# Kernel optimization log

Measured on AMD Instinct MI355X. Metric: run time of the kernel, lower is better.

The kernel has to match this reference:

```python
import jax, jax.numpy as jnp
import numpy as np

TYPE_NUM = 4
CHILDS = [2, 2, 2, 2]
NODE_NUM = 8          # sum(CHILDS)
HEADS = 4
GROUP = 4
IN, MID, OUT = 256, 256, 256


def _mask():
    m = np.zeros((TYPE_NUM, NODE_NUM), np.float32)
    s = 0
    for i, c in enumerate(CHILDS):
        m[i, s:s + c] = 1.0
        s += c
    return jnp.asarray(m)


def _graph_feature(x, node_num):
    # x: [B, L, C] -> [B, M, node_num+1, C] with M = (L-1)//node_num
    B, L, C = x.shape
    node_x = x[:, 1:, :].reshape(B, -1, C * node_num)
    M = node_x.shape[1]
    src = x[:, :M, :]
    return jnp.concatenate([node_x, src], axis=2).reshape(B, M, node_num + 1, C)


def _conv1d(x, w, b, groups):
    # x: [N, C, T], w: [O, C//groups, K], stride == K, 'VALID' -> length-1 output
    y = jax.lax.conv_general_dilated(
        x, w, window_strides=(w.shape[-1],), padding='VALID',
        feature_group_count=groups, dimension_numbers=('NCH', 'OIH', 'NCH'))
    return y + b[None, :, None]


def _agg(feat, attn, mask):
    # feat: [B, M, node_num+1, C]; attn: [B, M, node_num, HEADS] (softmaxed)
    B, M, A, C = feat.shape
    n = A - 1
    nf = feat[:, :, :-1, :].reshape(B, M, n, HEADS, C // HEADS) * attn[..., None]
    nf = nf.reshape(B, M, n, C)
    agg = jnp.einsum('tn,bmnc->bmtc', mask, nf)  # masked group-sum (bmm with block mask)
    return agg, feat[:, :, -1, :]


def setup_inputs() -> dict:
    key = jax.random.key(0)
    ks = jax.random.split(key, 12)
    B, L = 4, 32777

    def lin(k, fi, fo):
        return jax.random.normal(k, (fi, fo), jnp.float32) / np.sqrt(fi).astype(np.float32)

    def convw(k, o, i, kk):
        return jax.random.normal(k, (o, i, kk), jnp.float32) / np.sqrt(i * kk).astype(np.float32)

    return {
        'input': jax.random.normal(ks[0], (B, L, IN), jnp.float32),
        'gt': jax.random.normal(ks[1], (B, 512, IN), jnp.float32),
        'w_att': lin(ks[2], IN, HEADS), 'b_att': jnp.zeros((HEADS,), jnp.float32),
        'w_gt1': lin(ks[3], IN, MID), 'b_gt1': jnp.zeros((MID,), jnp.float32),
        'w_gt2': lin(ks[4], MID, OUT), 'b_gt2': jnp.zeros((OUT,), jnp.float32),
        'w_agg1': convw(ks[5], MID, IN // GROUP, TYPE_NUM), 'b_agg1': jnp.zeros((MID,), jnp.float32),
        'w_src1': convw(ks[6], MID, IN // GROUP, 1), 'b_src1': jnp.zeros((MID,), jnp.float32),
        'w_agg2': convw(ks[7], OUT, MID // GROUP, TYPE_NUM), 'b_agg2': jnp.zeros((OUT,), jnp.float32),
        'w_src2': convw(ks[8], OUT, MID // GROUP, 1), 'b_src2': jnp.zeros((OUT,), jnp.float32),
    }


def reference(input, gt, w_att, b_att, w_gt1, b_gt1, w_gt2, b_gt2,
              w_agg1, b_agg1, w_src1, b_src1, w_agg2, b_agg2, w_src2, b_src2):
    mask = _mask()
    B = gt.shape[0]
    # gt branch (eval mode: dropout = identity)
    gt1 = jax.nn.relu(gt @ w_gt1 + b_gt1)   # [B, 512, MID]
    gt2 = jax.nn.relu(gt1 @ w_gt2 + b_gt2)  # [B, 512, OUT]

    # ---- layer 1 ----
    feat = _graph_feature(input, NODE_NUM)   # [B, M, 9, IN]
    M = feat.shape[1]
    ft = feat[:, :, -1:, :] + feat[:, :, :-1, :]          # source + each neighbor
    attn = jax.nn.softmax(ft @ w_att + b_att, axis=2)     # softmax over node dim
    node, src = _agg(feat, attn, mask)                    # [B,M,T,IN], [B,M,IN]
    BM = B * M
    node = jnp.transpose(node.reshape(BM, TYPE_NUM, IN), (0, 2, 1))  # [BM, IN, T]
    src = src.reshape(BM, IN, 1)
    node1 = jax.nn.relu(_conv1d(node, w_agg1, b_agg1, GROUP))[:, :, 0]  # [BM, MID]
    src1 = jax.nn.relu(_conv1d(src, w_src1, b_src1, GROUP))[:, :, 0]

    nf1 = node1.reshape(B, M, MID)[:, 0, :]
    d1 = gt1[:, 0, :] - nf1
    score1 = 1.0 - jnp.exp(-0.5 * jnp.sum(d1 * d1, axis=1))  # [B]

    out1 = (node1 + src1).reshape(B, M, MID)

    # ---- layer 2 (reuses attn truncated to M2) ----
    feat2 = _graph_feature(out1, NODE_NUM)  # [B, M2, 9, MID]
    M2 = feat2.shape[1]
    node2, src2 = _agg(feat2, attn[:, :M2], mask)
    BM2 = B * M2
    node2 = jnp.transpose(node2.reshape(BM2, TYPE_NUM, MID), (0, 2, 1))
    src2 = src2.reshape(BM2, MID, 1)
    node2c = jax.nn.relu(_conv1d(node2, w_agg2, b_agg2, GROUP))  # [BM2, OUT, 1]

    nf2 = node2c.reshape(B, M2, OUT)
    d2 = (gt2[:, :M2, :] - nf2).reshape(-1, OUT)
    score2 = 1.0 - jnp.exp(-0.5 * jnp.sum(d2 * d2, axis=1))  # [B*M2]

    src2c = jax.nn.relu(_conv1d(src2, w_src2, b_src2, GROUP))
    output = (node2c + src2c).reshape(-1, OUT)  # [B*M2, OUT]
    return output, score1, score2
```

## Files before the change

kernel.cpp:

```cpp
#include <hip/hip_runtime.h>
#include <hip/hip_bf16.h>

typedef unsigned short u16;
typedef unsigned int   u32;
typedef __attribute__((ext_vector_type(8))) short short8;
typedef __attribute__((ext_vector_type(4))) float f32x4;

#define BB  4
#define LL  32777
#define MM  4097
#define MMP 4112
#define MM2 512

__device__ __forceinline__ float b2f(u16 u) { return __uint_as_float(((u32)u) << 16); }
__device__ __forceinline__ u16 f2bf(float f) {
    u32 u = __float_as_uint(f);
    return (u16)((u + 0x7fffu + ((u >> 16) & 1u)) >> 16);
}
__device__ __forceinline__ u32 pk(float a, float b) {
    union { __hip_bfloat162 h; u32 u; } cv;
    cv.h = __float22bfloat162_rn(make_float2(a, b));
    return cv.u;
}
__device__ __forceinline__ float bflo(u32 u) { return __uint_as_float(u << 16); }
__device__ __forceinline__ float bfhi(u32 u) { return __uint_as_float(u & 0xffff0000u); }

__global__ __launch_bounds__(256) void setup_k(
    const float* __restrict__ wagg1, const float* __restrict__ wagg2,
    const float* __restrict__ wsrc1, const float* __restrict__ wsrc2,
    const float* __restrict__ watt,
    u16* __restrict__ wA1, u16* __restrict__ wA2,
    u16* __restrict__ wS1, u16* __restrict__ wS2, u16* __restrict__ wattB) {
    int idx = blockIdx.x * 256 + threadIdx.x;
    if (idx < 131072) {
        int which = idx >> 16;
        int e = idx & 65535;
        int j = e & 7, lane = (e >> 3) & 63, mt = (e >> 9) & 3, kc = (e >> 11) & 7, g = (e >> 14) & 3;
        int ol = mt * 16 + (lane & 15);
        int k = kc * 32 + (lane >> 4) * 8 + j;
        int t = k >> 6, ci = k & 63;
        const float* src = which ? wagg2 : wagg1;
        u16* dst = which ? wA2 : wA1;
        dst[e] = f2bf(src[(g * 64 + ol) * 256 + ci * 4 + t]);
    } else if (idx < 163840) {
        int e2 = idx - 131072;
        int which = e2 >> 14;
        int e = e2 & 16383;
        int j = e & 7, lane = (e >> 3) & 63, mt = (e >> 9) & 3, kc = (e >> 11) & 1, g = (e >> 12) & 3;
        int ol = mt * 16 + (lane & 15);
        int k = kc * 32 + (lane >> 4) * 8 + j;
        const float* src = which ? wsrc2 : wsrc1;
        u16* dst = which ? wS2 : wS1;
        dst[e] = f2bf(src[(g * 64 + ol) * 64 + k]);
    } else {
        int e = idx - 163840;
        int j = e & 7, lane = (e >> 3) & 63, kc = e >> 9;
        int h = lane & 15, quad = lane >> 4;
        int k = kc * 32 + quad * 8 + j;
        wattB[e] = (h < 4) ? f2bf(watt[k * 4 + h]) : (u16)0;
    }
}

__global__ __launch_bounds__(256, 4) void l1fused_k(
    const float* __restrict__ x, const float* __restrict__ batt,
    const u16* __restrict__ wA1, const u16* __restrict__ wS1,
    const u16* __restrict__ wattB,
    const float* __restrict__ bagg1, const float* __restrict__ bsrc1,
    float* __restrict__ attnf, u16* __restrict__ out1, float* __restrict__ n1m0,
    const float* __restrict__ gt, const float* __restrict__ W1, const float* __restrict__ b1,
    const float* __restrict__ W2, const float* __restrict__ b2,
    float* __restrict__ gt2, float* __restrict__ gt1m0) {
    __shared__ u16   sh_node[64 * 256];
    __shared__ u16   sh_srcq[8 * 256];
    __shared__ float shR[320];

    int tid = threadIdx.x;
    int b = blockIdx.y;

    if (blockIdx.x < 64) {
        float (*sh)[8] = (float(*)[8])sh_node;
        int gi = blockIdx.x * 4 + b;
        int row0 = gi * 8;
        {
            int r = tid >> 5, j = tid & 31;
            const float4* a4 = (const float4*)(gt + (size_t)(row0 + r) * 256 + j * 8);
            float4 v0 = a4[0], v1 = a4[1];
            sh[j * 8 + 0][r] = v0.x; sh[j * 8 + 1][r] = v0.y;
            sh[j * 8 + 2][r] = v0.z; sh[j * 8 + 3][r] = v0.w;
            sh[j * 8 + 4][r] = v1.x; sh[j * 8 + 5][r] = v1.y;
            sh[j * 8 + 6][r] = v1.z; sh[j * 8 + 7][r] = v1.w;
        }
        __syncthreads();
        int o = tid;
        float acc[8];
        {
            float bo = b1[o];
            #pragma unroll
            for (int i = 0; i < 8; ++i) acc[i] = bo;
        }
        #pragma unroll 8
        for (int k = 0; k < 256; ++k) {
            float wv = W1[k * 256 + o];
            const float4* ap = (const float4*)&sh[k][0];
            float4 a0 = ap[0], a1 = ap[1];
            acc[0] = fmaf(a0.x, wv, acc[0]); acc[1] = fmaf(a0.y, wv, acc[1]);
            acc[2] = fmaf(a0.z, wv, acc[2]); acc[3] = fmaf(a0.w, wv, acc[3]);
            acc[4] = fmaf(a1.x, wv, acc[4]); acc[5] = fmaf(a1.y, wv, acc[5]);
            acc[6] = fmaf(a1.z, wv, acc[6]); acc[7] = fmaf(a1.w, wv, acc[7]);
        }
        #pragma unroll
        for (int i = 0; i < 8; ++i) acc[i] = fmaxf(acc[i], 0.f);
        if ((row0 & 511) == 0) gt1m0[(row0 >> 9) * 256 + o] = acc[0];
        __syncthreads();
        #pragma unroll
        for (int i = 0; i < 8; ++i) sh[o][i] = acc[i];
        __syncthreads();
        {
            float bo = b2[o];
            #pragma unroll
            for (int i = 0; i < 8; ++i) acc[i] = bo;
        }
        #pragma unroll 8
        for (int k = 0; k < 256; ++k) {
            float wv = W2[k * 256 + o];
            const float4* ap = (const float4*)&sh[k][0];
            float4 a0 = ap[0], a1 = ap[1];
            acc[0] = fmaf(a0.x, wv, acc[0]); acc[1] = fmaf(a0.y, wv, acc[1]);
            acc[2] = fmaf(a0.z, wv, acc[2]); acc[3] = fmaf(a0.w, wv, acc[3]);
            acc[4] = fmaf(a1.x, wv, acc[4]); acc[5] = fmaf(a1.y, wv, acc[5]);
            acc[6] = fmaf(a1.z, wv, acc[6]); acc[7] = fmaf(a1.w, wv, acc[7]);
        }
        #pragma unroll
        for (int i = 0; i < 8; ++i) gt2[(size_t)(row0 + i) * 256 + o] = fmaxf(acc[i], 0.f);
        return;
    }

    int bx = blockIdx.x - 64;
    int lane = tid & 63, w = tid >> 6;
    int quad = lane >> 4;
    int p0 = bx * 8;

    {
        int rslot = tid >> 4, cseg = tid & 15;
        const float* xb = x + (size_t)b * LL * 256;
        const float* srcA[5];
        u16* dstA[5];
        int keyA[5];
        #pragma unroll
        for (int pass = 0; pass < 5; ++pass) {
            int r = pass * 16 + rslot;
            int grow, key; u16* dst;
            if (r < 64) {
                int pos = r >> 3, nn = r & 7;
                int gp = p0 + pos; int gpc = gp < MM ? gp : MM - 1;
                grow = 1 + 8 * gpc + nn;
                dst = sh_node + r * 256;
                key = (pos ^ nn) & 7;
            } else {
                int q = r - 64;
                int qq = q < 8 ? q : 7;
                int gp = p0 + qq; int gpc = gp < MM ? gp : MM - 1;
                grow = gpc;
                dst = sh_srcq + qq * 256;
                key = qq & 7;
            }
            srcA[pass] = xb + (size_t)grow * 256 + cseg * 16;
            dstA[pass] = dst;
            keyA[pass] = key;
        }
        float4 v0[5], v1[5], v2[5], v3[5];
        #pragma unroll
        for (int pass = 0; pass < 5; ++pass) {
            asm volatile("global_load_dwordx4 %0, %1, off"           : "=v"(v0[pass]) : "v"(srcA[pass]));
            asm volatile("global_load_dwordx4 %0, %1, off offset:16" : "=v"(v1[pass]) : "v"(srcA[pass]));
            asm volatile("global_load_dwordx4 %0, %1, off offset:32" : "=v"(v2[pass]) : "v"(srcA[pass]));
            asm volatile("global_load_dwordx4 %0, %1, off offset:48" : "=v"(v3[pass]) : "v"(srcA[pass]));
        }
        asm volatile("s_waitcnt vmcnt(0)" ::: "memory");
        __builtin_amdgcn_sched_barrier(0);
        #pragma unroll
        for (int pass = 0; pass < 5; ++pass) {
            bool val = (pass < 4) || (rslot < 8);
            if (val) {
                uint4 o0, o1;
                o0.x = pk(v0[pass].x, v0[pass].y); o0.y = pk(v0[pass].z, v0[pass].w);
                o0.z = pk(v1[pass].x, v1[pass].y); o0.w = pk(v1[pass].z, v1[pass].w);
                o1.x = pk(v2[pass].x, v2[pass].y); o1.y = pk(v2[pass].z, v2[pass].w);
                o1.z = pk(v3[pass].x, v3[pass].y); o1.w = pk(v3[pass].z, v3[pass].w);
                int cb0 = cseg * 2, key = keyA[pass];
                *(uint4*)(dstA[pass] + ((cb0 ^ key) * 8))       = o0;
                *(uint4*)(dstA[pass] + (((cb0 + 1) ^ key) * 8)) = o1;
            }
        }
    }
    short8 wB[8];
    #pragma unroll
    for (int kc = 0; kc < 8; ++kc) wB[kc] = *(const short8*)(wattB + kc * 512 + lane * 8);
    float battw = batt[w];
    __syncthreads();

    {
        int m = lane & 15;
        int h = lane & 15;
        {
            int r = w * 16 + m;
            int key = ((r >> 3) ^ (r & 7)) & 7;
            const u16* rowp = sh_node + r * 256;
            f32x4 acc = (f32x4){0.f, 0.f, 0.f, 0.f};
            #pragma unroll
            for (int kc = 0; kc < 8; ++kc) {
                int cb = kc * 4 + quad;
                short8 aF = *(const short8*)(rowp + ((cb ^ key) * 8));
                acc = __builtin_amdgcn_mfma_f32_16x16x32_bf16(aF, wB[kc], acc, 0, 0, 0);
            }
            if (h < 4) {
                #pragma unroll
                for (int r2 = 0; r2 < 4; ++r2)
                    shR[(w * 16 + quad * 4 + r2) * 4 + h] = acc[r2];
            }
        }
        if (w == 3) {
            int ms = m < 8 ? m : 7;
            int key = ms & 7;
            const u16* rowp = sh_srcq + ms * 256;
            f32x4 acc = (f32x4){0.f, 0.f, 0.f, 0.f};
            #pragma unroll
            for (int kc = 0; kc < 8; ++kc) {
                int cb = kc * 4 + quad;
                short8 aF = *(const short8*)(rowp + ((cb ^ key) * 8));
                acc = __builtin_amdgcn_mfma_f32_16x16x32_bf16(aF, wB[kc], acc, 0, 0, 0);
            }
            if (h < 4) {
                #pragma unroll
                for (int r2 = 0; r2 < 4; ++r2) {
                    int rr = quad * 4 + r2;
                    if (rr < 8) shR[256 + rr * 4 + h] = acc[r2];
                }
            }
        }
    }
    __syncthreads();

    int g = w;
    int col = lane & 15;
    int pos = col & 7;
    float aT[8];
    {
        float base = shR[256 + pos * 4 + g] + battw;
        float l[8], mx = -3.0e38f;
        #pragma unroll
        for (int n = 0; n < 8; ++n) { l[n] = shR[(pos * 8 + n) * 4 + g] + base; mx = fmaxf(mx, l[n]); }
        float s = 0.f;
        #pragma unroll
        for (int n = 0; n < 8; ++n) { l[n] = __expf(l[n] - mx); s += l[n]; }
        float inv = 1.f / s;
        #pragma unroll
        for (int n = 0; n < 8; ++n) aT[n] = l[n] * inv;
        int gp = p0 + pos;
        if (quad == 0 && col < 8 && gp < MM2) {
            #pragma unroll
            for (int n = 0; n < 8; ++n)
                attnf[(((size_t)b * MM2 + gp) * 8 + n) * 4 + g] = aT[n];
        }
    }
    f32x4 accn[4], accs[4];
    #pragma unroll
    for (int mt = 0; mt < 4; ++mt) { accn[mt] = (f32x4){0,0,0,0}; accs[mt] = (f32x4){0,0,0,0}; }

    const u16* wAb = wA1 + (size_t)(g * 8) * 4 * 512 + lane * 8;
    short8 aAc[4];
    #pragma unroll
    for (int mt = 0; mt < 4; ++mt) aAc[mt] = *(const short8*)(wAb + mt * 512);

    #pragma unroll
    for (int kc = 0; kc < 8; ++kc) {
        short8 aAn[4];
        if (kc < 7) {
            #pragma unroll
            for (int mt = 0; mt < 4; ++mt) aAn[mt] = *(const short8*)(wAb + ((kc + 1) * 4 + mt) * 512);
        }
        int k0 = kc * 32 + quad * 8;
        int t = k0 >> 6, ci0 = k0 & 63;
        int cb = (g * 64 + ci0) >> 3;
        int r0 = pos * 8 + 2 * t;
        int key0 = (pos ^ (2 * t)) & 7, key1 = (pos ^ (2 * t + 1)) & 7;
        short8 n0 = *(const short8*)(sh_node + r0 * 256 + ((cb ^ key0) * 8));
        short8 n1 = *(const short8*)(sh_node + (r0 + 1) * 256 + ((cb ^ key1) * 8));
        float a0 = aT[2 * t], a1 = aT[2 * t + 1];
        union { uint4 u; short8 s; } cv;
        #pragma unroll
        for (int e = 0; e < 4; ++e) {
            float lo = fmaf(a0, b2f((u16)n0[2 * e]),     a1 * b2f((u16)n1[2 * e]));
            float hi = fmaf(a0, b2f((u16)n0[2 * e + 1]), a1 * b2f((u16)n1[2 * e + 1]));
            ((u32*)&cv.u)[e] = pk(lo, hi);
        }
        short8 bB = cv.s;
        #pragma unroll
        for (int mt = 0; mt < 4; ++mt)
            accn[mt] = __builtin_amdgcn_mfma_f32_16x16x32_bf16(aAc[mt], bB, accn[mt], 0, 0, 0);
        if (kc < 7) {
            #pragma unroll
            for (int mt = 0; mt < 4; ++mt) aAc[mt] = aAn[mt];
        }
    }
    #pragma unroll
    for (int kc = 0; kc < 2; ++kc) {
        int cb = (g * 64 + kc * 32 + quad * 8) >> 3;
        short8 bS = *(const short8*)(sh_srcq + pos * 256 + ((cb ^ pos) * 8));
        #pragma unroll
        for (int mt = 0; mt < 4; ++mt) {
            short8 aS = *(const short8*)(wS1 + (((g * 2 + kc) * 4 + mt) * 512 + lane * 8));
            accs[mt] = __builtin_amdgcn_mfma_f32_16x16x32_bf16(aS, bS, accs[mt], 0, 0, 0);
        }
    }
    __syncthreads();

    u16* outt = sh_srcq;
    #pragma unroll
    for (int mt = 0; mt < 4; ++mt) {
        int ob = g * 64 + mt * 16 + quad * 4;
        float v[4], n1v[4];
        #pragma unroll
        for (int r = 0; r < 4; ++r) {
            int o = ob + r;
            float n1 = fmaxf(accn[mt][r] + bagg1[o], 0.f);
            float s1 = fmaxf(accs[mt][r] + bsrc1[o], 0.f);
            n1v[r] = n1;
            v[r] = n1 + s1;
        }
        if (col < 8) {
            u32* wp = (u32*)&outt[col * 256 + ob];
            wp[0] = pk(v[0], v[1]);
            wp[1] = pk(v[2], v[3]);
        }
        if (bx == 0 && col == 0) {
            #pragma unroll
            for (int r = 0; r < 4; ++r) n1m0[b * 256 + ob + r] = n1v[r];
        }
    }
    __syncthreads();
    {
        int posw = tid >> 5, cc = (tid & 31) * 8;
        if (p0 + posw < MM)
            *(uint4*)&out1[((size_t)b * MMP + p0 + posw) * 256 + cc] = *(const uint4*)&outt[posw * 256 + cc];
    }
}

__global__ __launch_bounds__(256) void l2conv_k(
    const u16* __restrict__ out1, const float* __restrict__ attnf,
    const float* __restrict__ gt2,
    const u16* __restrict__ wA2, const u16* __restrict__ wS2,
    const float* __restrict__ bagg2, const float* __restrict__ bsrc2,
    const float* __restrict__ gt1m0, const float* __restrict__ n1m0,
    float* __restrict__ outp, float* __restrict__ score2p, float* __restrict__ score1p) {
    __shared__ char shraw[16 * 268 * 4 * 2];
    __shared__ float shred[128];

    int tid = threadIdx.x;
    int b = blockIdx.y;

    if (blockIdx.x == 128) {
        float d = gt1m0[b * 256 + tid] - n1m0[b * 256 + tid];
        float v = d * d;
        #pragma unroll
        for (int off = 32; off > 0; off >>= 1) v += __shfl_down(v, off, 64);
        if ((tid & 63) == 0) shred[tid >> 6] = v;
        __syncthreads();
        if (tid == 0) score1p[b] = 1.f - __expf(-0.5f * (shred[0] + shred[1] + shred[2] + shred[3]));
        return;
    }

    int p0 = blockIdx.x * 4;
    u16* aggl = (u16*)shraw;

    {
        int pos16 = tid >> 4, cc = tid & 15;
        int pos = pos16 & 3;
        int m = p0 + pos;
        int c0 = cc * 16;
        int h = c0 >> 6;
        const float* arow = attnf + ((size_t)b * MM2 + m) * 32;
        uint4 P0[4], P1[4], Q0[4], Q1[4];
        float a0v[4], a1v[4];
        #pragma unroll
        for (int t = 0; t < 4; ++t) {
            const uint4* r0 = (const uint4*)(out1 + ((size_t)b * MMP + 1 + 8 * m + 2 * t) * 256 + c0);
            const uint4* r1 = (const uint4*)(out1 + ((size_t)b * MMP + 2 + 8 * m + 2 * t) * 256 + c0);
            P0[t] = r0[0]; P1[t] = r0[1];
            Q0[t] = r1[0]; Q1[t] = r1[1];
            a0v[t] = arow[(2 * t) * 4 + h];
            a1v[t] = arow[(2 * t + 1) * 4 + h];
        }
        #pragma unroll
        for (int t = 0; t < 4; ++t) {
            float a0 = a0v[t], a1 = a1v[t];
            u32 w[8];
            {
                u32 pv[4] = {P0[t].x, P0[t].y, P0[t].z, P0[t].w};
                u32 qv[4] = {Q0[t].x, Q0[t].y, Q0[t].z, Q0[t].w};
                #pragma unroll
                for (int e = 0; e < 4; ++e) {
                    float lo = fmaf(bflo(pv[e]), a0, bflo(qv[e]) * a1);
                    float hi = fmaf(bfhi(pv[e]), a0, bfhi(qv[e]) * a1);
                    w[e] = pk(lo, hi);
                }
            }
            {
                u32 pv[4] = {P1[t].x, P1[t].y, P1[t].z, P1[t].w};
                u32 qv[4] = {Q1[t].x, Q1[t].y, Q1[t].z, Q1[t].w};
                #pragma unroll
                for (int e = 0; e < 4; ++e) {
                    float lo = fmaf(bflo(pv[e]), a0, bflo(qv[e]) * a1);
                    float hi = fmaf(bfhi(pv[e]), a0, bfhi(qv[e]) * a1);
                    w[4 + e] = pk(lo, hi);
                }
            }
            u32* dst = (u32*)&aggl[pos16 * 1024 + h * 256 + t * 64 + (c0 & 63)];
            ((uint4*)dst)[0] = make_uint4(w[0], w[1], w[2], w[3]);
            ((uint4*)dst)[1] = make_uint4(w[4], w[5], w[6], w[7]);
        }
    }
    __syncthreads();

    int lane = tid & 63, g = tid >> 6;
    int col = lane & 15, quad = lane >> 4;
    f32x4 accn[4], accs[4];
    #pragma unroll
    for (int mt = 0; mt < 4; ++mt) { accn[mt] = (f32x4){0,0,0,0}; accs[mt] = (f32x4){0,0,0,0}; }

    const u16* wAb = wA2 + (size_t)(g * 8) * 4 * 512 + lane * 8;
    short8 aAc[4];
    #pragma unroll
    for (int mt = 0; mt < 4; ++mt) aAc[mt] = *(const short8*)(wAb + mt * 512);

    #pragma unroll
    for (int kc = 0; kc < 8; ++kc) {
        short8 aAn[4];
        if (kc < 7) {
            #pragma unroll
            for (int mt = 0; mt < 4; ++mt) aAn[mt] = *(const short8*)(wAb + ((kc + 1) * 4 + mt) * 512);
        }
        short8 bB = *(const short8*)&aggl[col * 1024 + g * 256 + kc * 32 + quad * 8];
        #pragma unroll
        for (int mt = 0; mt < 4; ++mt)
            accn[mt] = __builtin_amdgcn_mfma_f32_16x16x32_bf16(aAc[mt], bB, accn[mt], 0, 0, 0);
        if (kc < 7) {
            #pragma unroll
            for (int mt = 0; mt < 4; ++mt) aAc[mt] = aAn[mt];
        }
    }
    {
        int pcol = col & 3;
        #pragma unroll
        for (int kc = 0; kc < 2; ++kc) {
            short8 bS = *(const short8*)(out1 + ((size_t)b * MMP + p0 + pcol) * 256 + g * 64 + kc * 32 + quad * 8);
            #pragma unroll
            for (int mt = 0; mt < 4; ++mt) {
                short8 aS = *(const short8*)(wS2 + (((g * 2 + kc) * 4 + mt) * 512 + lane * 8));
                accs[mt] = __builtin_amdgcn_mfma_f32_16x16x32_bf16(aS, bS, accs[mt], 0, 0, 0);
            }
        }
    }
    __syncthreads();

    float* outt = (float*)shraw;
    float* n2t  = outt + 16 * 268;
    #pragma unroll
    for (int mt = 0; mt < 4; ++mt) {
        #pragma unroll
        for (int r = 0; r < 4; ++r) {
            int o = g * 64 + mt * 16 + quad * 4 + r;
            float n2 = fmaxf(accn[mt][r] + bagg2[o], 0.f);
            float s2 = fmaxf(accs[mt][r] + bsrc2[o], 0.f);
            outt[col * 268 + o] = n2 + s2;
            n2t[col * 268 + o] = n2;
        }
    }
    __syncthreads();

    {
        int pos = tid >> 6, cc = (tid & 63) * 4;
        *(float4*)&outp[((size_t)b * MM2 + p0 + pos) * 256 + cc] = *(const float4*)&outt[pos * 268 + cc];
    }
    if (tid < 64) {
        int pos = tid >> 4, kk = tid & 15;
        const float* grow = gt2 + ((size_t)b * MM2 + p0 + pos) * 256 + kk * 16;
        const float* nrow = n2t + pos * 268 + kk * 16;
        float s = 0.f;
        #pragma unroll
        for (int c = 0; c < 16; ++c) { float d = grow[c] - nrow[c]; s = fmaf(d, d, s); }
        shred[pos * 16 + kk] = s;
    }
    __syncthreads();
    if (tid < 4) {
        float s = 0.f;
        #pragma unroll
        for (int kk = 0; kk < 16; ++kk) s += shred[tid * 16 + kk];
        score2p[(size_t)b * MM2 + p0 + tid] = 1.f - __expf(-0.5f * s);
    }
}

extern "C" void kernel_launch(void* const* d_in, const int* in_sizes, int n_in,
                              void* d_out, int out_size, void* d_ws, size_t ws_size,
                              hipStream_t stream) {
    const float* x     = (const float*)d_in[0];
    const float* gt    = (const float*)d_in[1];
    const float* watt  = (const float*)d_in[2];
    const float* batt  = (const float*)d_in[3];
    const float* wgt1  = (const float*)d_in[4];
    const float* bgt1  = (const float*)d_in[5];
    const float* wgt2  = (const float*)d_in[6];
    const float* bgt2  = (const float*)d_in[7];
    const float* wagg1 = (const float*)d_in[8];
    const float* bagg1 = (const float*)d_in[9];
    const float* wsrc1 = (const float*)d_in[10];
    const float* bsrc1 = (const float*)d_in[11];
    const float* wagg2 = (const float*)d_in[12];
    const float* bagg2 = (const float*)d_in[13];
    const float* wsrc2 = (const float*)d_in[14];
    const float* bsrc2 = (const float*)d_in[15];

    char* ws = (char*)d_ws;
    float* ws_gt2  = (float*)(ws + 0);
    float* attnf   = (float*)(ws + 2097152);
    float* n1m0    = (float*)(ws + 2359296);
    float* gt1m0   = (float*)(ws + 2363392);
    u16*   wA1     = (u16*)(ws + 2367488);
    u16*   wS1     = (u16*)(ws + 2498560);
    u16*   wA2     = (u16*)(ws + 2531328);
    u16*   wS2     = (u16*)(ws + 2662400);
    u16*   wattB   = (u16*)(ws + 2695168);
    u16*   out1    = (u16*)(ws + 2703360);

    float* outp    = (float*)d_out;
    float* score1p = outp + 524288;
    float* score2p = outp + 524292;

    setup_k<<<dim3(656), dim3(256), 0, stream>>>(wagg1, wagg2, wsrc1, wsrc2, watt,
                                                 wA1, wA2, wS1, wS2, wattB);
    l1fused_k<<<dim3(577, 4), dim3(256), 0, stream>>>(x, batt, wA1, wS1, wattB, bagg1, bsrc1,
                                                      attnf, out1, n1m0,
                                                      gt, wgt1, bgt1, wgt2, bgt2, ws_gt2, gt1m0);
    l2conv_k<<<dim3(129, 4), dim3(256), 0, stream>>>(out1, attnf, ws_gt2, wA2, wS2, bagg2, bsrc2,
                                                     gt1m0, n1m0, outp, score2p, score1p);
}
```

Before: 249.1 us.

## Make layer-1 blocks persistent over two tiles with prefetched next-tile loads

The layer-1 kernel grid shrinks from 577 to 321 blocks per batch. Each of the first 256 compute blocks now handles two position tiles (tile and tile+257), and it issues the global loads for the second tile during the first tile's MFMA work so load latency overlaps compute. Launch bounds drop to 3 waves per SIMD to make room for the extra live registers, and the gt MLP loops are unrolled further. The cost is lower occupancy, extra barriers, and an uneven load in which some blocks do one tile and others do two.

```diff
diff --git a/kernel.cpp b/kernel.cpp
--- a/kernel.cpp
+++ b/kernel.cpp
@@ -61,7 +61,79 @@
     }
 }
 
-__global__ __launch_bounds__(256, 4) void l1fused_k(
+__device__ __forceinline__ void stage_addr(int p0i, int r, int& grow, int& key, bool& val, int& lr) {
+    if (r < 64) {
+        int pos = r >> 3, nn = r & 7;
+        int gp = p0i + pos; int gpc = gp < MM ? gp : MM - 1;
+        grow = 1 + 8 * gpc + nn;
+        key = (pos ^ nn) & 7;
+        val = true; lr = r;
+    } else {
+        int q = r - 64; int qq = q < 8 ? q : 7;
+        int gp = p0i + qq; int gpc = gp < MM ? gp : MM - 1;
+        grow = gpc;
+        key = qq & 7;
+        val = (q < 8); lr = qq;
+    }
+}
+
+__device__ __forceinline__ void stage_issue_asm(const float* xb, int p0i, int rslot, int cseg,
+                                                float4* v0, float4* v1, float4* v2, float4* v3) {
+    #pragma unroll
+    for (int pass = 0; pass < 5; ++pass) {
+        int grow, key, lr; bool val;
+        stage_addr(p0i, pass * 16 + rslot, grow, key, val, lr);
+        const float* sp = xb + (size_t)grow * 256 + cseg * 16;
+        asm volatile("global_load_dwordx4 %0, %1, off"           : "=v"(v0[pass]) : "v"(sp));
+        asm volatile("global_load_dwordx4 %0, %1, off offset:16" : "=v"(v1[pass]) : "v"(sp));
+        asm volatile("global_load_dwordx4 %0, %1, off offset:32" : "=v"(v2[pass]) : "v"(sp));
+        asm volatile("global_load_dwordx4 %0, %1, off offset:48" : "=v"(v3[pass]) : "v"(sp));
+    }
+}
+
+__device__ __forceinline__ void stage_issue_cpp(const float* xb, int p0i, int rslot, int cseg,
+                                                float4* v0, float4* v1, float4* v2, float4* v3) {
+    #pragma unroll
+    for (int pass = 0; pass < 5; ++pass) {
+        int grow, key, lr; bool val;
+        stage_addr(p0i, pass * 16 + rslot, grow, key, val, lr);
+        const float4* sp = (const float4*)(xb + (size_t)grow * 256 + cseg * 16);
+        v0[pass] = sp[0]; v1[pass] = sp[1]; v2[pass] = sp[2]; v3[pass] = sp[3];
+    }
+}
+
+__device__ __forceinline__ void stage_write(u16* sh_node, u16* sh_srcq, int rslot, int cseg,
+                                            const float4* v0, const float4* v1,
+                                            const float4* v2, const float4* v3) {
+    #pragma unroll
+    for (int pass = 0; pass < 5; ++pass) {
+        int r = pass * 16 + rslot;
+        u16* dst; int key; bool val = true;
+        if (r < 64) {
+            int pos = r >> 3, nn = r & 7;
+            dst = sh_node + r * 256;
+            key = (pos ^ nn) & 7;
+        } else {
+            int q = r - 64;
+            val = (q < 8);
+            int qq = q < 8 ? q : 7;
+            dst = sh_srcq + qq * 256;
+            key = qq & 7;
+        }
+        if (val) {
+            uint4 o0, o1;
+            o0.x = pk(v0[pass].x, v0[pass].y); o0.y = pk(v0[pass].z, v0[pass].w);
+            o0.z = pk(v1[pass].x, v1[pass].y); o0.w = pk(v1[pass].z, v1[pass].w);
+            o1.x = pk(v2[pass].x, v2[pass].y); o1.y = pk(v2[pass].z, v2[pass].w);
+            o1.z = pk(v3[pass].x, v3[pass].y); o1.w = pk(v3[pass].z, v3[pass].w);
+            int cb0 = cseg * 2;
+            *(uint4*)(dst + ((cb0 ^ key) * 8))       = o0;
+            *(uint4*)(dst + (((cb0 + 1) ^ key) * 8)) = o1;
+        }
+    }
+}
+
+__global__ __launch_bounds__(256, 3) void l1fused_k(
     const float* __restrict__ x, const float* __restrict__ batt,
     const u16* __restrict__ wA1, const u16* __restrict__ wS1,
     const u16* __restrict__ wattB,
@@ -98,7 +170,7 @@
             #pragma unroll
             for (int i = 0; i < 8; ++i) acc[i] = bo;
         }
-        #pragma unroll 8
+        #pragma unroll 16
         for (int k = 0; k < 256; ++k) {
             float wv = W1[k * 256 + o];
             const float4* ap = (const float4*)&sh[k][0];
@@ -120,7 +192,7 @@
             #pragma unroll
             for (int i = 0; i < 8; ++i) acc[i] = bo;
         }
-        #pragma unroll 8
+        #pragma unroll 16
         for (int k = 0; k < 256; ++k) {
             float wv = W2[k * 256 + o];
             const float4* ap = (const float4*)&sh[k][0];
@@ -135,214 +207,179 @@
         return;
     }
 
-    int bx = blockIdx.x - 64;
+    int bxb = blockIdx.x - 64;
+    int nt = (bxb < 256) ? 2 : 1;
     int lane = tid & 63, w = tid >> 6;
     int quad = lane >> 4;
-    int p0 = bx * 8;
-
-    {
-        int rslot = tid >> 4, cseg = tid & 15;
-        const float* xb = x + (size_t)b * LL * 256;
-        const float* srcA[5];
-        u16* dstA[5];
-        int keyA[5];
-        #pragma unroll
-        for (int pass = 0; pass < 5; ++pass) {
-            int r = pass * 16 + rslot;
-            int grow, key; u16* dst;
-            if (r < 64) {
-                int pos = r >> 3, nn = r & 7;
-                int gp = p0 + pos; int gpc = gp < MM ? gp : MM - 1;
-                grow = 1 + 8 * gpc + nn;
-                dst = sh_node + r * 256;
-                key = (pos ^ nn) & 7;
-            } else {
-                int q = r - 64;
-                int qq = q < 8 ? q : 7;
-                int gp = p0 + qq; int gpc = gp < MM ? gp : MM - 1;
-                grow = gpc;
-                dst = sh_srcq + qq * 256;
-                key = qq & 7;
-            }
-            srcA[pass] = xb + (size_t)grow * 256 + cseg * 16;
-            dstA[pass] = dst;
-            keyA[pass] = key;
-        }
-        float4 v0[5], v1[5], v2[5], v3[5];
-        #pragma unroll
-        for (int pass = 0; pass < 5; ++pass) {
-            asm volatile("global_load_dwordx4 %0, %1, off"           : "=v"(v0[pass]) : "v"(srcA[pass]));
-            asm volatile("global_load_dwordx4 %0, %1, off offset:16" : "=v"(v1[pass]) : "v"(srcA[pass]));
-            asm volatile("global_load_dwordx4 %0, %1, off offset:32" : "=v"(v2[pass]) : "v"(srcA[pass]));
-            asm volatile("global_load_dwordx4 %0, %1, off offset:48" : "=v"(v3[pass]) : "v"(srcA[pass]));
-        }
-        asm volatile("s_waitcnt vmcnt(0)" ::: "memory");
-        __builtin_amdgcn_sched_barrier(0);
-        #pragma unroll
-        for (int pass = 0; pass < 5; ++pass) {
-            bool val = (pass < 4) || (rslot < 8);
-            if (val) {
-                uint4 o0, o1;
-                o0.x = pk(v0[pass].x, v0[pass].y); o0.y = pk(v0[pass].z, v0[pass].w);
-                o0.z = pk(v1[pass].x, v1[pass].y); o0.w = pk(v1[pass].z, v1[pass].w);
-                o1.x = pk(v2[pass].x, v2[pass].y); o1.y = pk(v2[pass].z, v2[pass].w);
-                o1.z = pk(v3[pass].x, v3[pass].y); o1.w = pk(v3[pass].z, v3[pass].w);
-                int cb0 = cseg * 2, key = keyA[pass];
-                *(uint4*)(dstA[pass] + ((cb0 ^ key) * 8))       = o0;
-                *(uint4*)(dstA[pass] + (((cb0 + 1) ^ key) * 8)) = o1;
-            }
-        }
-    }
-    short8 wB[8];
-    #pragma unroll
-    for (int kc = 0; kc < 8; ++kc) wB[kc] = *(const short8*)(wattB + kc * 512 + lane * 8);
+    int rslot = tid >> 4, cseg = tid & 15;
+    const float* xb = x + (size_t)b * LL * 256;
     float battw = batt[w];
-    __syncthreads();
-
-    {
-        int m = lane & 15;
-        int h = lane & 15;
-        {
-            int r = w * 16 + m;
-            int key = ((r >> 3) ^ (r & 7)) & 7;
-            const u16* rowp = sh_node + r * 256;
-            f32x4 acc = (f32x4){0.f, 0.f, 0.f, 0.f};
-            #pragma unroll
-            for (int kc = 0; kc < 8; ++kc) {
-                int cb = kc * 4 + quad;
-                short8 aF = *(const short8*)(rowp + ((cb ^ key) * 8));
-                acc = __builtin_amdgcn_mfma_f32_16x16x32_bf16(aF, wB[kc], acc, 0, 0, 0);
-            }
-            if (h < 4) {
-                #pragma unroll
-                for (int r2 = 0; r2 < 4; ++r2)
-                    shR[(w * 16 + quad * 4 + r2) * 4 + h] = acc[r2];
-            }
-        }
-        if (w == 3) {
-            int ms = m < 8 ? m : 7;
-            int key = ms & 7;
-            const u16* rowp = sh_srcq + ms * 256;
-            f32x4 acc = (f32x4){0.f, 0.f, 0.f, 0.f};
-            #pragma unroll
-            for (int kc = 0; kc < 8; ++kc) {
-                int cb = kc * 4 + quad;
-                short8 aF = *(const short8*)(rowp + ((cb ^ key) * 8));
-                acc = __builtin_amdgcn_mfma_f32_16x16x32_bf16(aF, wB[kc], acc, 0, 0, 0);
-            }
-            if (h < 4) {
-                #pragma unroll
-                for (int r2 = 0; r2 < 4; ++r2) {
-                    int rr = quad * 4 + r2;
-                    if (rr < 8) shR[256 + rr * 4 + h] = acc[r2];
-                }
-            }
-        }
-    }
+
+    float4 v0[5], v1[5], v2[5], v3[5];
+
+    stage_issue_asm(xb, bxb * 8, rslot, cseg, v0, v1, v2, v3);
+    asm volatile("s_waitcnt vmcnt(0)" ::: "memory");
+    __builtin_amdgcn_sched_barrier(0);
+    stage_write(sh_node, sh_srcq, rslot, cseg, v0, v1, v2, v3);
     __syncthreads();
 
     int g = w;
     int col = lane & 15;
     int pos = col & 7;
-    float aT[8];
-    {
-        float base = shR[256 + pos * 4 + g] + battw;
-        float l[8], mx = -3.0e38f;
-        #pragma unroll
-        for (int n = 0; n < 8; ++n) { l[n] = shR[(pos * 8 + n) * 4 + g] + base; mx = fmaxf(mx, l[n]); }
-        float s = 0.f;
-        #pragma unroll
-        for (int n = 0; n < 8; ++n) { l[n] = __expf(l[n] - mx); s += l[n]; }
-        float inv = 1.f / s;
-        #pragma unroll
-        for (int n = 0; n < 8; ++n) aT[n] = l[n] * inv;
-        int gp = p0 + pos;
-        if (quad == 0 && col < 8 && gp < MM2) {
-            #pragma unroll
-            for (int n = 0; n < 8; ++n)
-                attnf[(((size_t)b * MM2 + gp) * 8 + n) * 4 + g] = aT[n];
-        }
-    }
-    f32x4 accn[4], accs[4];
-    #pragma unroll
-    for (int mt = 0; mt < 4; ++mt) { accn[mt] = (f32x4){0,0,0,0}; accs[mt] = (f32x4){0,0,0,0}; }
-
-    const u16* wAb = wA1 + (size_t)(g * 8) * 4 * 512 + lane * 8;
-    short8 aAc[4];
-    #pragma unroll
-    for (int mt = 0; mt < 4; ++mt) aAc[mt] = *(const short8*)(wAb + mt * 512);
-
-    #pragma unroll
-    for (int kc = 0; kc < 8; ++kc) {
-        short8 aAn[4];
-        if (kc < 7) {
-            #pragma unroll
-            for (int mt = 0; mt < 4; ++mt) aAn[mt] = *(const short8*)(wAb + ((kc + 1) * 4 + mt) * 512);
-        }
-        int k0 = kc * 32 + quad * 8;
-        int t = k0 >> 6, ci0 = k0 & 63;
-        int cb = (g * 64 + ci0) >> 3;
-        int r0 = pos * 8 + 2 * t;
-        int key0 = (pos ^ (2 * t)) & 7, key1 = (pos ^ (2 * t + 1)) & 7;
-        short8 n0 = *(const short8*)(sh_node + r0 * 256 + ((cb ^ key0) * 8));
-        short8 n1 = *(const short8*)(sh_node + (r0 + 1) * 256 + ((cb ^ key1) * 8));
-        float a0 = aT[2 * t], a1 = aT[2 * t + 1];
-        union { uint4 u; short8 s; } cv;
-        #pragma unroll
-        for (int e = 0; e < 4; ++e) {
-            float lo = fmaf(a0, b2f((u16)n0[2 * e]),     a1 * b2f((u16)n1[2 * e]));
-            float hi = fmaf(a0, b2f((u16)n0[2 * e + 1]), a1 * b2f((u16)n1[2 * e + 1]));
-            ((u32*)&cv.u)[e] = pk(lo, hi);
-        }
-        short8 bB = cv.s;
-        #pragma unroll
-        for (int mt = 0; mt < 4; ++mt)
-            accn[mt] = __builtin_amdgcn_mfma_f32_16x16x32_bf16(aAc[mt], bB, accn[mt], 0, 0, 0);
-        if (kc < 7) {
-            #pragma unroll
-            for (int mt = 0; mt < 4; ++mt) aAc[mt] = aAn[mt];
-        }
-    }
-    #pragma unroll
-    for (int kc = 0; kc < 2; ++kc) {
-        int cb = (g * 64 + kc * 32 + quad * 8) >> 3;
-        short8 bS = *(const short8*)(sh_srcq + pos * 256 + ((cb ^ pos) * 8));
+
+    for (int ti = 0; ti < nt; ++ti) {
+        int tile = bxb + ti * 257;
+        int p0 = tile * 8;
+        bool pre = (ti + 1 < nt);
+
+        short8 wB[8];
+        #pragma unroll
+        for (int kc = 0; kc < 8; ++kc) wB[kc] = *(const short8*)(wattB + kc * 512 + lane * 8);
+        {
+            int m = lane & 15;
+            int h = lane & 15;
+            {
+                int r = w * 16 + m;
+                int key = ((r >> 3) ^ (r & 7)) & 7;
+                const u16* rowp = sh_node + r * 256;
+                f32x4 acc = (f32x4){0.f, 0.f, 0.f, 0.f};
+                #pragma unroll
+                for (int kc = 0; kc < 8; ++kc) {
+                    int cb = kc * 4 + quad;
+                    short8 aF = *(const short8*)(rowp + ((cb ^ key) * 8));
+                    acc = __builtin_amdgcn_mfma_f32_16x16x32_bf16(aF, wB[kc], acc, 0, 0, 0);
+                }
+                if (h < 4) {
+                    #pragma unroll
+                    for (int r2 = 0; r2 < 4; ++r2)
+                        shR[(w * 16 + quad * 4 + r2) * 4 + h] = acc[r2];
+                }
+            }
+            if (w == 3) {
+                int ms = m < 8 ? m : 7;
+                int key = ms & 7;
+                const u16* rowp = sh_srcq + ms * 256;
+                f32x4 acc = (f32x4){0.f, 0.f, 0.f, 0.f};
+                #pragma unroll
+                for (int kc = 0; kc < 8; ++kc) {
+                    int cb = kc * 4 + quad;
+                    short8 aF = *(const short8*)(rowp + ((cb ^ key) * 8));
+                    acc = __builtin_amdgcn_mfma_f32_16x16x32_bf16(aF, wB[kc], acc, 0, 0, 0);
+                }
+                if (h < 4) {
+                    #pragma unroll
+                    for (int r2 = 0; r2 < 4; ++r2) {
+                        int rr = quad * 4 + r2;
+                        if (rr < 8) shR[256 + rr * 4 + h] = acc[r2];
+                    }
+                }
+            }
+        }
+        __syncthreads();
+
+        float aT[8];
+        {
+            float base = shR[256 + pos * 4 + g] + battw;
+            float l[8], mx = -3.0e38f;
+            #pragma unroll
+            for (int n = 0; n < 8; ++n) { l[n] = shR[(pos * 8 + n) * 4 + g] + base; mx = fmaxf(mx, l[n]); }
+            float s = 0.f;
+            #pragma unroll
+            for (int n = 0; n < 8; ++n) { l[n] = __expf(l[n] - mx); s += l[n]; }
+            float inv = 1.f / s;
+            #pragma unroll
+            for (int n = 0; n < 8; ++n) aT[n] = l[n] * inv;
+            int gp = p0 + pos;
+            if (quad == 0 && col < 8 && gp < MM2) {
+                #pragma unroll
+                for (int n = 0; n < 8; ++n)
+                    attnf[(((size_t)b * MM2 + gp) * 8 + n) * 4 + g] = aT[n];
+            }
+        }
+
+        f32x4 accn[4];
+        #pragma unroll
+        for (int mt = 0; mt < 4; ++mt) accn[mt] = (f32x4){0, 0, 0, 0};
+        const u16* wAb = wA1 + (size_t)(g * 8) * 4 * 512 + lane * 8;
+        #pragma unroll
+        for (int kc = 0; kc < 8; ++kc) {
+            int k0 = kc * 32 + quad * 8;
+            int t = k0 >> 6, ci0 = k0 & 63;
+            int cb = (g * 64 + ci0) >> 3;
+            int r0 = pos * 8 + 2 * t;
+            int key0 = (pos ^ (2 * t)) & 7, key1 = (pos ^ (2 * t + 1)) & 7;
+            short8 n0 = *(const short8*)(sh_node + r0 * 256 + ((cb ^ key0) * 8));
+            short8 n1 = *(const short8*)(sh_node + (r0 + 1) * 256 + ((cb ^ key1) * 8));
+            float a0 = aT[2 * t], a1 = aT[2 * t + 1];
+            union { uint4 u; short8 s; } cv;
+            #pragma unroll
+            for (int e = 0; e < 4; ++e) {
+                float lo = fmaf(a0, b2f((u16)n0[2 * e]),     a1 * b2f((u16)n1[2 * e]));
+                float hi = fmaf(a0, b2f((u16)n0[2 * e + 1]), a1 * b2f((u16)n1[2 * e + 1]));
+                ((u32*)&cv.u)[e] = pk(lo, hi);
+            }
+            short8 bB = cv.s;
+            #pragma unroll
+            for (int mt = 0; mt < 4; ++mt) {
+                short8 aA = *(const short8*)(wAb + (kc * 4 + mt) * 512);
+                accn[mt] = __builtin_amdgcn_mfma_f32_16x16x32_bf16(aA, bB, accn[mt], 0, 0, 0);
+            }
+        }
+
+        if (pre) {
+            stage_issue_cpp(xb, (bxb + (ti + 1) * 257) * 8, rslot, cseg, v0, v1, v2, v3);
+            __builtin_amdgcn_sched_barrier(0);
+        }
+
+        f32x4 accs[4];
+        #pragma unroll
+        for (int mt = 0; mt < 4; ++mt) accs[mt] = (f32x4){0, 0, 0, 0};
+        #pragma unroll
+        for (int kc = 0; kc < 2; ++kc) {
+            int cb = (g * 64 + kc * 32 + quad * 8) >> 3;
+            short8 bS = *(const short8*)(sh_srcq + pos * 256 + ((cb ^ pos) * 8));
+            #pragma unroll
+            for (int mt = 0; mt < 4; ++mt) {
+                short8 aS = *(const short8*)(wS1 + (((g * 2 + kc) * 4 + mt) * 512 + lane * 8));
+                accs[mt] = __builtin_amdgcn_mfma_f32_16x16x32_bf16(aS, bS, accs[mt], 0, 0, 0);
+            }
+        }
+        __syncthreads();
+
+        u16* outt = sh_srcq;
         #pragma unroll
         for (int mt = 0; mt < 4; ++mt) {
-            short8 aS = *(const short8*)(wS1 + (((g * 2 + kc) * 4 + mt) * 512 + lane * 8));
-            accs[mt] = __builtin_amdgcn_mfma_f32_16x16x32_bf16(aS, bS, accs[mt], 0, 0, 0);
-        }
-    }
-    __syncthreads();
-
-    u16* outt = sh_srcq;
-    #pragma unroll
-    for (int mt = 0; mt < 4; ++mt) {
-        int ob = g * 64 + mt * 16 + quad * 4;
-        float v[4], n1v[4];
-        #pragma unroll
-        for (int r = 0; r < 4; ++r) {
-            int o = ob + r;
-            float n1 = fmaxf(accn[mt][r] + bagg1[o], 0.f);
-            float s1 = fmaxf(accs[mt][r] + bsrc1[o], 0.f);
-            n1v[r] = n1;
-            v[r] = n1 + s1;
-        }
-        if (col < 8) {
-            u32* wp = (u32*)&outt[col * 256 + ob];
-            wp[0] = pk(v[0], v[1]);
-            wp[1] = pk(v[2], v[3]);
-        }
-        if (bx == 0 && col == 0) {
-            #pragma unroll
-            for (int r = 0; r < 4; ++r) n1m0[b * 256 + ob + r] = n1v[r];
-        }
-    }
-    __syncthreads();
-    {
-        int posw = tid >> 5, cc = (tid & 31) * 8;
-        if (p0 + posw < MM)
-            *(uint4*)&out1[((size_t)b * MMP + p0 + posw) * 256 + cc] = *(const uint4*)&outt[posw * 256 + cc];
+            int ob = g * 64 + mt * 16 + quad * 4;
+            float v[4], n1v[4];
+            #pragma unroll
+            for (int r = 0; r < 4; ++r) {
+                int o = ob + r;
+                float n1 = fmaxf(accn[mt][r] + bagg1[o], 0.f);
+                float s1 = fmaxf(accs[mt][r] + bsrc1[o], 0.f);
+                n1v[r] = n1;
+                v[r] = n1 + s1;
+            }
+            if (col < 8) {
+                u32* wp = (u32*)&outt[col * 256 + ob];
+                wp[0] = pk(v[0], v[1]);
+                wp[1] = pk(v[2], v[3]);
+            }
+            if (tile == 0 && col == 0) {
+                #pragma unroll
+                for (int r = 0; r < 4; ++r) n1m0[b * 256 + ob + r] = n1v[r];
+            }
+        }
+        __syncthreads();
+        {
+            int posw = tid >> 5, cc = (tid & 31) * 8;
+            if (p0 + posw < MM)
+                *(uint4*)&out1[((size_t)b * MMP + p0 + posw) * 256 + cc] = *(const uint4*)&outt[posw * 256 + cc];
+        }
+        if (pre) {
+            __syncthreads();
+            stage_write(sh_node, sh_srcq, rslot, cseg, v0, v1, v2, v3);
+            __syncthreads();
+        }
     }
 }
 
@@ -538,7 +575,7 @@
 
     setup_k<<<dim3(656), dim3(256), 0, stream>>>(wagg1, wagg2, wsrc1, wsrc2, watt,
                                                  wA1, wA2, wS1, wS2, wattB);
-    l1fused_k<<<dim3(577, 4), dim3(256), 0, stream>>>(x, batt, wA1, wS1, wattB, bagg1, bsrc1,
+    l1fused_k<<<dim3(321, 4), dim3(256), 0, stream>>>(x, batt, wA1, wS1, wattB, bagg1, bsrc1,
                                                       attnf, out1, n1m0,
                                                       gt, wgt1, bgt1, wgt2, bgt2, ws_gt2, gt1m0);
     l2conv_k<<<dim3(129, 4), dim3(256), 0, stream>>>(out1, attnf, ws_gt2, wA2, wS2, bagg2, bsrc2,
```

Result: slower. 478.1 us (+91.9%).

## Halve layer-1 positions per block to raise occupancy and block count

Applied to the files above, without the earlier changes.

The fused layer-1 kernel now handles 4 positions per block instead of 8. This halves LDS use and doubles the grid (1089 blocks per batch), and the launch bound rises to 6 blocks per SM. The hand-written batched asm loads with an explicit wait are replaced by plain loads, and the weight prefetch double-buffer in the MFMA loop is removed to free registers. The cost is that half the waves idle in the epilogue and MFMA B columns, and the weights are reloaded by twice as many blocks.

```diff
diff --git a/kernel.cpp b/kernel.cpp
--- a/kernel.cpp
+++ b/kernel.cpp
@@ -61,7 +61,7 @@
     }
 }
 
-__global__ __launch_bounds__(256, 4) void l1fused_k(
+__global__ __launch_bounds__(256, 6) void l1fused_k(
     const float* __restrict__ x, const float* __restrict__ batt,
     const u16* __restrict__ wA1, const u16* __restrict__ wS1,
     const u16* __restrict__ wattB,
@@ -70,9 +70,9 @@
     const float* __restrict__ gt, const float* __restrict__ W1, const float* __restrict__ b1,
     const float* __restrict__ W2, const float* __restrict__ b2,
     float* __restrict__ gt2, float* __restrict__ gt1m0) {
-    __shared__ u16   sh_node[64 * 256];
-    __shared__ u16   sh_srcq[8 * 256];
-    __shared__ float shR[320];
+    __shared__ u16   sh_node[32 * 256];
+    __shared__ u16   sh_srcq[4 * 256];
+    __shared__ float shR[144];
 
     int tid = threadIdx.x;
     int b = blockIdx.y;
@@ -98,7 +98,7 @@
             #pragma unroll
             for (int i = 0; i < 8; ++i) acc[i] = bo;
         }
-        #pragma unroll 8
+        #pragma unroll 16
         for (int k = 0; k < 256; ++k) {
             float wv = W1[k * 256 + o];
             const float4* ap = (const float4*)&sh[k][0];
@@ -120,7 +120,7 @@
             #pragma unroll
             for (int i = 0; i < 8; ++i) acc[i] = bo;
         }
-        #pragma unroll 8
+        #pragma unroll 16
         for (int k = 0; k < 256; ++k) {
             float wv = W2[k * 256 + o];
             const float4* ap = (const float4*)&sh[k][0];
@@ -138,50 +138,46 @@
     int bx = blockIdx.x - 64;
     int lane = tid & 63, w = tid >> 6;
     int quad = lane >> 4;
-    int p0 = bx * 8;
+    int p0 = bx * 4;
 
     {
         int rslot = tid >> 4, cseg = tid & 15;
         const float* xb = x + (size_t)b * LL * 256;
-        const float* srcA[5];
-        u16* dstA[5];
-        int keyA[5];
-        #pragma unroll
-        for (int pass = 0; pass < 5; ++pass) {
+        const float4* sp[3];
+        u16* dstA[3];
+        int keyA[3];
+        bool valA[3];
+        #pragma unroll
+        for (int pass = 0; pass < 3; ++pass) {
             int r = pass * 16 + rslot;
-            int grow, key; u16* dst;
-            if (r < 64) {
+            int grow, key; u16* dst; bool val = true;
+            if (r < 32) {
                 int pos = r >> 3, nn = r & 7;
                 int gp = p0 + pos; int gpc = gp < MM ? gp : MM - 1;
                 grow = 1 + 8 * gpc + nn;
+                key = (pos ^ nn) & 7;
                 dst = sh_node + r * 256;
-                key = (pos ^ nn) & 7;
             } else {
-                int q = r - 64;
-                int qq = q < 8 ? q : 7;
+                int q = r - 32;
+                val = (q < 4);
+                int qq = q < 4 ? q : 3;
                 int gp = p0 + qq; int gpc = gp < MM ? gp : MM - 1;
                 grow = gpc;
+                key = qq;
                 dst = sh_srcq + qq * 256;
-                key = qq & 7;
-            }
-            srcA[pass] = xb + (size_t)grow * 256 + cseg * 16;
-            dstA[pass] = dst;
-            keyA[pass] = key;
-        }
-        float4 v0[5], v1[5], v2[5], v3[5];
-        #pragma unroll
-        for (int pass = 0; pass < 5; ++pass) {
-            asm volatile("global_load_dwordx4 %0, %1, off"           : "=v"(v0[pass]) : "v"(srcA[pass]));
-            asm volatile("global_load_dwordx4 %0, %1, off offset:16" : "=v"(v1[pass]) : "v"(srcA[pass]));
-            asm volatile("global_load_dwordx4 %0, %1, off offset:32" : "=v"(v2[pass]) : "v"(srcA[pass]));
-            asm volatile("global_load_dwordx4 %0, %1, off offset:48" : "=v"(v3[pass]) : "v"(srcA[pass]));
-        }
-        asm volatile("s_waitcnt vmcnt(0)" ::: "memory");
-        __builtin_amdgcn_sched_barrier(0);
-        #pragma unroll
-        for (int pass = 0; pass < 5; ++pass) {
-            bool val = (pass < 4) || (rslot < 8);
-            if (val) {
+            }
+            sp[pass] = (const float4*)(xb + (size_t)grow * 256 + cseg * 16);
+            dstA[pass] = dst; keyA[pass] = key; valA[pass] = val;
+        }
+        float4 v0[3], v1[3], v2[3], v3[3];
+        #pragma unroll
+        for (int pass = 0; pass < 3; ++pass) {
+            v0[pass] = sp[pass][0]; v1[pass] = sp[pass][1];
+            v2[pass] = sp[pass][2]; v3[pass] = sp[pass][3];
+        }
+        #pragma unroll
+        for (int pass = 0; pass < 3; ++pass) {
+            if (valA[pass]) {
                 uint4 o0, o1;
                 o0.x = pk(v0[pass].x, v0[pass].y); o0.y = pk(v0[pass].z, v0[pass].w);
                 o0.z = pk(v1[pass].x, v1[pass].y); o0.w = pk(v1[pass].z, v1[pass].w);
@@ -202,7 +198,7 @@
     {
         int m = lane & 15;
         int h = lane & 15;
-        {
+        if (w < 2) {
             int r = w * 16 + m;
             int key = ((r >> 3) ^ (r & 7)) & 7;
             const u16* rowp = sh_node + r * 256;
@@ -218,10 +214,9 @@
                 for (int r2 = 0; r2 < 4; ++r2)
                     shR[(w * 16 + quad * 4 + r2) * 4 + h] = acc[r2];
             }
-        }
-        if (w == 3) {
-            int ms = m < 8 ? m : 7;
-            int key = ms & 7;
+        } else if (w == 2) {
+            int ms = m < 4 ? m : 3;
+            int key = ms;
             const u16* rowp = sh_srcq + ms * 256;
             f32x4 acc = (f32x4){0.f, 0.f, 0.f, 0.f};
             #pragma unroll
@@ -234,7 +229,7 @@
                 #pragma unroll
                 for (int r2 = 0; r2 < 4; ++r2) {
                     int rr = quad * 4 + r2;
-                    if (rr < 8) shR[256 + rr * 4 + h] = acc[r2];
+                    if (rr < 4) shR[128 + rr * 4 + h] = acc[r2];
                 }
             }
         }
@@ -243,10 +238,10 @@
 
     int g = w;
     int col = lane & 15;
-    int pos = col & 7;
+    int pos = col & 3;
     float aT[8];
     {
-        float base = shR[256 + pos * 4 + g] + battw;
+        float base = shR[128 + pos * 4 + g] + battw;
         float l[8], mx = -3.0e38f;
         #pragma unroll
         for (int n = 0; n < 8; ++n) { l[n] = shR[(pos * 8 + n) * 4 + g] + base; mx = fmaxf(mx, l[n]); }
@@ -257,28 +252,19 @@
         #pragma unroll
         for (int n = 0; n < 8; ++n) aT[n] = l[n] * inv;
         int gp = p0 + pos;
-        if (quad == 0 && col < 8 && gp < MM2) {
+        if (quad == 0 && col < 4 && gp < MM2) {
             #pragma unroll
             for (int n = 0; n < 8; ++n)
                 attnf[(((size_t)b * MM2 + gp) * 8 + n) * 4 + g] = aT[n];
         }
     }
-    f32x4 accn[4], accs[4];
-    #pragma unroll
-    for (int mt = 0; mt < 4; ++mt) { accn[mt] = (f32x4){0,0,0,0}; accs[mt] = (f32x4){0,0,0,0}; }
-
+
+    f32x4 accn[4];
+    #pragma unroll
+    for (int mt = 0; mt < 4; ++mt) accn[mt] = (f32x4){0, 0, 0, 0};
     const u16* wAb = wA1 + (size_t)(g * 8) * 4 * 512 + lane * 8;
-    short8 aAc[4];
-    #pragma unroll
-    for (int mt = 0; mt < 4; ++mt) aAc[mt] = *(const short8*)(wAb + mt * 512);
-
     #pragma unroll
     for (int kc = 0; kc < 8; ++kc) {
-        short8 aAn[4];
-        if (kc < 7) {
-            #pragma unroll
-            for (int mt = 0; mt < 4; ++mt) aAn[mt] = *(const short8*)(wAb + ((kc + 1) * 4 + mt) * 512);
-        }
         int k0 = kc * 32 + quad * 8;
         int t = k0 >> 6, ci0 = k0 & 63;
         int cb = (g * 64 + ci0) >> 3;
@@ -296,13 +282,14 @@
         }
         short8 bB = cv.s;
         #pragma unroll
-        for (int mt = 0; mt < 4; ++mt)
-            accn[mt] = __builtin_amdgcn_mfma_f32_16x16x32_bf16(aAc[mt], bB, accn[mt], 0, 0, 0);
-        if (kc < 7) {
-            #pragma unroll
-            for (int mt = 0; mt < 4; ++mt) aAc[mt] = aAn[mt];
-        }
-    }
+        for (int mt = 0; mt < 4; ++mt) {
+            short8 aA = *(const short8*)(wAb + (kc * 4 + mt) * 512);
+            accn[mt] = __builtin_amdgcn_mfma_f32_16x16x32_bf16(aA, bB, accn[mt], 0, 0, 0);
+        }
+    }
+    f32x4 accs[4];
+    #pragma unroll
+    for (int mt = 0; mt < 4; ++mt) accs[mt] = (f32x4){0, 0, 0, 0};
     #pragma unroll
     for (int kc = 0; kc < 2; ++kc) {
         int cb = (g * 64 + kc * 32 + quad * 8) >> 3;
@@ -328,7 +315,7 @@
             n1v[r] = n1;
             v[r] = n1 + s1;
         }
-        if (col < 8) {
+        if (col < 4) {
             u32* wp = (u32*)&outt[col * 256 + ob];
             wp[0] = pk(v[0], v[1]);
             wp[1] = pk(v[2], v[3]);
@@ -339,7 +326,7 @@
         }
     }
     __syncthreads();
-    {
+    if (tid < 128) {
         int posw = tid >> 5, cc = (tid & 31) * 8;
         if (p0 + posw < MM)
             *(uint4*)&out1[((size_t)b * MMP + p0 + posw) * 256 + cc] = *(const uint4*)&outt[posw * 256 + cc];
@@ -538,9 +525,9 @@
 
     setup_k<<<dim3(656), dim3(256), 0, stream>>>(wagg1, wagg2, wsrc1, wsrc2, watt,
                                                  wA1, wA2, wS1, wS2, wattB);
-    l1fused_k<<<dim3(577, 4), dim3(256), 0, stream>>>(x, batt, wA1, wS1, wattB, bagg1, bsrc1,
-                                                      attnf, out1, n1m0,
-                                                      gt, wgt1, bgt1, wgt2, bgt2, ws_gt2, gt1m0);
+    l1fused_k<<<dim3(1089, 4), dim3(256), 0, stream>>>(x, batt, wA1, wS1, wattB, bagg1, bsrc1,
+                                                       attnf, out1, n1m0,
+                                                       gt, wgt1, bgt1, wgt2, bgt2, ws_gt2, gt1m0);
     l2conv_k<<<dim3(129, 4), dim3(256), 0, stream>>>(out1, attnf, ws_gt2, wA2, wS2, bagg2, bsrc2,
                                                      gt1m0, n1m0, outp, score2p, score1p);
 }
```

After: 260.2 us. 1.04x slower.
